# Performance work log

Measured on AMD Instinct MI355X. Metric: run time of the kernel, lower is better.

## Reference

```python
import jax, jax.numpy as jnp
import numpy as np

jax.config.update("jax_enable_x64", True)  # anchor_ids * 2654435761 needs int64, matching torch semantics

B, NV, D = 200000, 5, 64
CANTOR_DEPTH = 8
VOLUME_SCALE = 10.0
VOLUME_W, EDGE_W, SPREAD_W = 0.4, 0.3, 0.3
EPS = 1e-6
KNUTH = 2654435761


def setup_inputs() -> dict:
    key = jax.random.key(0)
    vertices = jax.random.normal(key, (B, NV, D), dtype=jnp.float32)
    anchor_ids = jnp.arange(B, dtype=jnp.int64)
    return {"vertices": vertices, "anchor_ids": anchor_ids}


def reference(vertices, anchor_ids):
    dtype = vertices.dtype
    b = vertices.shape[0]

    # pairwise squared distances between the 5 vertices: [B, 5, 5]
    diff = vertices[:, :, None, :] - vertices[:, None, :, :]
    dist_sq = (diff ** 2).sum(-1)

    # Cayley-Menger 6x6 matrix and 4-simplex volume
    M = jnp.zeros((b, 6, 6), dtype=dtype)
    M = M.at[:, 0, 1:].set(1.0)
    M = M.at[:, 1:, 0].set(1.0)
    M = M.at[:, 1:, 1:].set(dist_sq)
    det = jnp.linalg.det(M)
    volume = jnp.sqrt(jnp.clip(-det / 9216.0, 0.0))

    # edge statistics over the 10 unique edges (unbiased std, as torch.std)
    iu, ju = np.triu_indices(5, k=1)
    edges = jnp.sqrt(dist_sq[:, iu, ju])  # [B, 10]
    mean_edge = edges.mean(axis=1)
    std_edge = edges.std(axis=1, ddof=1)

    # vertex spread: std of distances to centroid (unbiased)
    centroid = vertices.mean(axis=1, keepdims=True)
    dists = jnp.linalg.norm(vertices - centroid, axis=-1)  # [B, 5]
    spread = dists.std(axis=1, ddof=1)

    volume_norm = jax.nn.sigmoid(volume * VOLUME_SCALE)
    edge_ratio = jax.nn.sigmoid(std_edge / (mean_edge + EPS))
    spread_norm = jax.nn.sigmoid(spread)
    seed = volume_norm * VOLUME_W + edge_ratio * EDGE_W + spread_norm * SPREAD_W

    # anchor id hash contribution (int64 modular arithmetic as in torch)
    id_contrib = ((anchor_ids.astype(jnp.int64) * KNUTH) % 1000000).astype(dtype) / 1000000.0
    seed = 0.1 * seed + 0.9 * id_contrib
    seed = jnp.clip(seed, EPS, 1.0 - EPS)

    # Cantor digit extraction (unrolled fixed-depth loop)
    x = seed
    cantor_val = jnp.zeros_like(x)
    factor = 0.5
    for _ in range(CANTOR_DEPTH):
        x_scaled = x * 3.0
        digit = x_scaled.astype(jnp.int32)  # trunc == floor for x >= 0
        x = x_scaled - digit.astype(dtype)
        cantor_val = cantor_val + (digit == 2).astype(dtype) * factor
        factor *= 0.5
    return jnp.clip(cantor_val, 0.0, 1.0)
```

## Files before the change

kernel.cpp:

```cpp
#include <hip/hip_runtime.h>
#include <stdint.h>


#define THREADS 256
#define ANCH_PER_BLOCK 256

__global__ __launch_bounds__(THREADS) void fingerprint_kernel(
    const float* __restrict__ vertices,
    const void* __restrict__ ids_raw,
    float* __restrict__ out,
    int n)
{
    __shared__ double stats[ANCH_PER_BLOCK][17];

    const int tid  = threadIdx.x;
    const int wave = tid >> 6;
    const int lane = tid & 63;
    const int g    = lane >> 2;
    const int r    = lane & 3;
    const int blockBase = blockIdx.x * ANCH_PER_BLOCK;

    #pragma unroll 1
    for (int it = 0; it < 4; ++it) {
        const int alocal = wave * 64 + it * 16 + g;
        int a = blockBase + alocal;
        int aload = (a < n) ? a : (n - 1);
        const float* vb = vertices + (size_t)aload * 320;

        double ip[15];
        #pragma unroll
        for (int p = 0; p < 15; ++p) ip[p] = 0.0;

        #pragma unroll
        for (int k = 0; k < 4; ++k) {
            float xv[5][4];
            #pragma unroll
            for (int v = 0; v < 5; ++v) {
                float4 t = *(const float4*)(vb + v * 64 + k * 16 + r * 4);
                xv[v][0] = t.x; xv[v][1] = t.y; xv[v][2] = t.z; xv[v][3] = t.w;
            }
            #pragma unroll
            for (int c = 0; c < 4; ++c) {
                double x[5];
                #pragma unroll
                for (int v = 0; v < 5; ++v) x[v] = (double)xv[v][c];
                int p = 0;
                #pragma unroll
                for (int v = 0; v < 5; ++v)
                    #pragma unroll
                    for (int w = v; w < 5; ++w) {
                        ip[p] = fma(x[v], x[w], ip[p]);
                        ++p;
                    }
            }
        }

        #pragma unroll
        for (int p = 0; p < 15; ++p) {
            ip[p] += __shfl_xor(ip[p], 1);
            ip[p] += __shfl_xor(ip[p], 2);
        }

        stats[alocal][r]     = ip[r];
        stats[alocal][4 + r] = ip[4 + r];
        stats[alocal][8 + r] = ip[8 + r];
        if (r < 3) stats[alocal][12 + r] = ip[12 + r];
    }

    __syncthreads();

    const int a = blockBase + tid;
    if (a >= n) return;

    double ip[15];
    #pragma unroll
    for (int p = 0; p < 15; ++p) ip[p] = stats[tid][p];

    const int IP[5][5] = {
        { 0, 1, 2, 3, 4},
        { 1, 5, 6, 7, 8},
        { 2, 6, 9,10,11},
        { 3, 7,10,12,13},
        { 4, 8,11,13,14}};

    double dsq[5][5];
    #pragma unroll
    for (int i = 0; i < 5; ++i) {
        dsq[i][i] = 0.0;
        #pragma unroll
        for (int j = i + 1; j < 5; ++j) {
            double d = ip[IP[i][i]] + ip[IP[j][j]] - 2.0 * ip[IP[i][j]];
            dsq[i][j] = d; dsq[j][i] = d;
        }
    }

    double esum = 0.0, e[10];
    {
        int p = 0;
        #pragma unroll
        for (int i = 0; i < 5; ++i)
            #pragma unroll
            for (int j = i + 1; j < 5; ++j) {
                e[p] = sqrt(dsq[i][j]); esum += e[p]; ++p;
            }
    }
    double emean = esum * 0.1;
    double evar = 0.0;
    #pragma unroll
    for (int p = 0; p < 10; ++p) { double d = e[p] - emean; evar += d * d; }
    double estd = sqrt(evar / 9.0);

    double rowsum[5], tot = 0.0;
    #pragma unroll
    for (int i = 0; i < 5; ++i) {
        double s = 0.0;
        #pragma unroll
        for (int w = 0; w < 5; ++w) s += ip[IP[i][w]];
        rowsum[i] = s; tot += s;
    }
    double c2 = tot * 0.04;
    double dsum = 0.0, dd[5];
    #pragma unroll
    for (int i = 0; i < 5; ++i) {
        double s2 = ip[IP[i][i]] - 0.4 * rowsum[i] + c2;
        dd[i] = sqrt(fmax(s2, 0.0)); dsum += dd[i];
    }
    double dmean = dsum * 0.2;
    double svar = 0.0;
    #pragma unroll
    for (int i = 0; i < 5; ++i) { double d = dd[i] - dmean; svar += d * d; }
    double spread = sqrt(svar * 0.25);

    double G[4][4];
    #pragma unroll
    for (int i = 0; i < 4; ++i)
        #pragma unroll
        for (int j = 0; j < 4; ++j)
            G[i][j] = 0.5 * (dsq[0][i + 1] + dsq[0][j + 1] - dsq[i + 1][j + 1]);

    double m01 = G[2][2] * G[3][3] - G[2][3] * G[3][2];
    double m02 = G[2][1] * G[3][3] - G[2][3] * G[3][1];
    double m03 = G[2][1] * G[3][2] - G[2][2] * G[3][1];
    double m04 = G[2][0] * G[3][3] - G[2][3] * G[3][0];
    double m05 = G[2][0] * G[3][2] - G[2][2] * G[3][0];
    double m06 = G[2][0] * G[3][1] - G[2][1] * G[3][0];
    double det =
        G[0][0] * (G[1][1] * m01 - G[1][2] * m02 + G[1][3] * m03)
      - G[0][1] * (G[1][0] * m01 - G[1][2] * m04 + G[1][3] * m05)
      + G[0][2] * (G[1][0] * m02 - G[1][1] * m04 + G[1][3] * m06)
      - G[0][3] * (G[1][0] * m03 - G[1][1] * m05 + G[1][2] * m06);

    double volume = sqrt(fmax(det / 576.0, 0.0));

    double vn = 1.0 / (1.0 + exp(-10.0 * volume));
    double er = 1.0 / (1.0 + exp(-(estd / (emean + 1e-6))));
    double sn = 1.0 / (1.0 + exp(-spread));
    double seed = 0.4 * vn + 0.3 * er + 0.3 * sn;

    const int* ai32 = (const int*)ids_raw;
    long long idv;
    if (ai32[1] == 0) {
        idv = ((const long long*)ids_raw)[a];
    } else {
        idv = (long long)ai32[a];
    }
    long long h = (idv * 2654435761LL) % 1000000LL;
    double idc = (double)h / 1000000.0;

    seed = 0.1 * seed + 0.9 * idc;
    seed = fmin(fmax(seed, 1e-6), 1.0 - 1e-6);

    double x = seed, cant = 0.0, factor = 0.5;
    #pragma unroll
    for (int itc = 0; itc < 8; ++itc) {
        double xs = x * 3.0;
        int dg = (int)xs;
        x = xs - (double)dg;
        cant += (dg == 2) ? factor : 0.0;
        factor *= 0.5;
    }
    out[a] = (float)fmin(fmax(cant, 0.0), 1.0);
}

extern "C" void kernel_launch(void* const* d_in, const int* in_sizes, int n_in,
                              void* d_out, int out_size, void* d_ws, size_t ws_size,
                              hipStream_t stream) {
    const float* vertices = (const float*)d_in[0];
    const void*  ids      = d_in[1];
    float* out = (float*)d_out;
    int n = in_sizes[1];
    int grid = (n + ANCH_PER_BLOCK - 1) / ANCH_PER_BLOCK;
    fingerprint_kernel<<<grid, THREADS, 0, stream>>>(vertices, ids, out, n);
}
```

Before: 354.3 us.

## Compute per-anchor epilogue redundantly in 4 lanes, drop shared-memory staging

Measured after the change: 414.4 us. +17.0%, slower.

```diff
diff --git a/kernel.cpp b/kernel.cpp
--- a/kernel.cpp
+++ b/kernel.cpp
@@ -3,78 +3,55 @@
 
 
 #define THREADS 256
-#define ANCH_PER_BLOCK 256
 
-__global__ __launch_bounds__(THREADS) void fingerprint_kernel(
+__global__ __launch_bounds__(THREADS, 4) void fingerprint_kernel(
     const float* __restrict__ vertices,
     const void* __restrict__ ids_raw,
     float* __restrict__ out,
     int n)
 {
-    __shared__ double stats[ANCH_PER_BLOCK][17];
+    const int tid  = threadIdx.x;
+    const int r    = tid & 3;
+    const int a    = blockIdx.x * (THREADS / 4) + (tid >> 2);
+    const int aload = (a < n) ? a : (n - 1);
+    const float* vb = vertices + (size_t)aload * 320;
 
-    const int tid  = threadIdx.x;
-    const int wave = tid >> 6;
-    const int lane = tid & 63;
-    const int g    = lane >> 2;
-    const int r    = lane & 3;
-    const int blockBase = blockIdx.x * ANCH_PER_BLOCK;
-
-    #pragma unroll 1
-    for (int it = 0; it < 4; ++it) {
-        const int alocal = wave * 64 + it * 16 + g;
-        int a = blockBase + alocal;
-        int aload = (a < n) ? a : (n - 1);
-        const float* vb = vertices + (size_t)aload * 320;
-
-        double ip[15];
-        #pragma unroll
-        for (int p = 0; p < 15; ++p) ip[p] = 0.0;
-
+    float xv[5][4][4];
+    #pragma unroll
+    for (int v = 0; v < 5; ++v)
         #pragma unroll
         for (int k = 0; k < 4; ++k) {
-            float xv[5][4];
-            #pragma unroll
-            for (int v = 0; v < 5; ++v) {
-                float4 t = *(const float4*)(vb + v * 64 + k * 16 + r * 4);
-                xv[v][0] = t.x; xv[v][1] = t.y; xv[v][2] = t.z; xv[v][3] = t.w;
-            }
-            #pragma unroll
-            for (int c = 0; c < 4; ++c) {
-                double x[5];
-                #pragma unroll
-                for (int v = 0; v < 5; ++v) x[v] = (double)xv[v][c];
-                int p = 0;
-                #pragma unroll
-                for (int v = 0; v < 5; ++v)
-                    #pragma unroll
-                    for (int w = v; w < 5; ++w) {
-                        ip[p] = fma(x[v], x[w], ip[p]);
-                        ++p;
-                    }
-            }
+            float4 t = *(const float4*)(vb + v * 64 + k * 16 + r * 4);
+            xv[v][k][0] = t.x; xv[v][k][1] = t.y;
+            xv[v][k][2] = t.z; xv[v][k][3] = t.w;
         }
-
-        #pragma unroll
-        for (int p = 0; p < 15; ++p) {
-            ip[p] += __shfl_xor(ip[p], 1);
-            ip[p] += __shfl_xor(ip[p], 2);
-        }
-
-        stats[alocal][r]     = ip[r];
-        stats[alocal][4 + r] = ip[4 + r];
-        stats[alocal][8 + r] = ip[8 + r];
-        if (r < 3) stats[alocal][12 + r] = ip[12 + r];
-    }
-
-    __syncthreads();
-
-    const int a = blockBase + tid;
-    if (a >= n) return;
 
     double ip[15];
     #pragma unroll
-    for (int p = 0; p < 15; ++p) ip[p] = stats[tid][p];
+    for (int p = 0; p < 15; ++p) ip[p] = 0.0;
+
+    #pragma unroll
+    for (int k = 0; k < 4; ++k)
+        #pragma unroll
+        for (int c = 0; c < 4; ++c) {
+            double x[5];
+            #pragma unroll
+            for (int v = 0; v < 5; ++v) x[v] = (double)xv[v][k][c];
+            int p = 0;
+            #pragma unroll
+            for (int v = 0; v < 5; ++v)
+                #pragma unroll
+                for (int w = v; w < 5; ++w) {
+                    ip[p] = fma(x[v], x[w], ip[p]);
+                    ++p;
+                }
+        }
+
+    #pragma unroll
+    for (int p = 0; p < 15; ++p) {
+        ip[p] += __shfl_xor(ip[p], 1);
+        ip[p] += __shfl_xor(ip[p], 2);
+    }
 
     const int IP[5][5] = {
         { 0, 1, 2, 3, 4},
@@ -83,25 +60,15 @@
         { 3, 7,10,12,13},
         { 4, 8,11,13,14}};
 
-    double dsq[5][5];
-    #pragma unroll
-    for (int i = 0; i < 5; ++i) {
-        dsq[i][i] = 0.0;
-        #pragma unroll
-        for (int j = i + 1; j < 5; ++j) {
-            double d = ip[IP[i][i]] + ip[IP[j][j]] - 2.0 * ip[IP[i][j]];
-            dsq[i][j] = d; dsq[j][i] = d;
-        }
-    }
-
-    double esum = 0.0, e[10];
+    double e[10], esum = 0.0;
     {
         int p = 0;
         #pragma unroll
         for (int i = 0; i < 5; ++i)
             #pragma unroll
             for (int j = i + 1; j < 5; ++j) {
-                e[p] = sqrt(dsq[i][j]); esum += e[p]; ++p;
+                double d = ip[IP[i][i]] + ip[IP[j][j]] - 2.0 * ip[IP[i][j]];
+                e[p] = sqrt(d); esum += e[p]; ++p;
             }
     }
     double emean = esum * 0.1;
@@ -136,7 +103,8 @@
     for (int i = 0; i < 4; ++i)
         #pragma unroll
         for (int j = 0; j < 4; ++j)
-            G[i][j] = 0.5 * (dsq[0][i + 1] + dsq[0][j + 1] - dsq[i + 1][j + 1]);
+            G[i][j] = ip[IP[0][0]] - ip[IP[0][i + 1]] - ip[IP[0][j + 1]]
+                    + ip[IP[i + 1][j + 1]];
 
     double m01 = G[2][2] * G[3][3] - G[2][3] * G[3][2];
     double m02 = G[2][1] * G[3][3] - G[2][3] * G[3][1];
@@ -160,9 +128,9 @@
     const int* ai32 = (const int*)ids_raw;
     long long idv;
     if (ai32[1] == 0) {
-        idv = ((const long long*)ids_raw)[a];
+        idv = ((const long long*)ids_raw)[aload];
     } else {
-        idv = (long long)ai32[a];
+        idv = (long long)ai32[aload];
     }
     long long h = (idv * 2654435761LL) % 1000000LL;
     double idc = (double)h / 1000000.0;
@@ -179,7 +147,9 @@
         cant += (dg == 2) ? factor : 0.0;
         factor *= 0.5;
     }
-    out[a] = (float)fmin(fmax(cant, 0.0), 1.0);
+
+    if (r == 0 && a < n)
+        out[a] = (float)fmin(fmax(cant, 0.0), 1.0);
 }
 
 extern "C" void kernel_launch(void* const* d_in, const int* in_sizes, int n_in,
@@ -189,6 +159,7 @@
     const void*  ids      = d_in[1];
     float* out = (float*)d_out;
     int n = in_sizes[1];
-    int grid = (n + ANCH_PER_BLOCK - 1) / ANCH_PER_BLOCK;
+    int anchorsPerBlock = THREADS / 4;
+    int grid = (n + anchorsPerBlock - 1) / anchorsPerBlock;
     fingerprint_kernel<<<grid, THREADS, 0, stream>>>(vertices, ids, out, n);
 }
```
